# Kernel tuning notes

Measured on AMD Instinct MI355X. Metric: run time of the kernel, lower is better.

## Reference

```python
import math
import jax, jax.numpy as jnp
import numpy as np

BATCH, SEQ, EMBED, HEADS = 2, 2048, 1024, 16
HEAD_DIM = EMBED // HEADS


def setup_inputs() -> dict:
    key = jax.random.key(0)
    k1, k2, k3 = jax.random.split(key, 3)
    scale = 1.0 / math.sqrt(EMBED)  # keep pre-softmax logits in a sane range
    x = jax.random.normal(k1, (BATCH, SEQ, EMBED), dtype=jnp.float32)
    mask = jnp.ones((BATCH, SEQ), dtype=jnp.int32)
    qkv_w = jax.random.normal(k2, (3 * EMBED, EMBED), dtype=jnp.float32) * scale
    out_w = jax.random.normal(k3, (EMBED, EMBED), dtype=jnp.float32) * scale
    out_b = jnp.zeros((EMBED,), dtype=jnp.float32)
    return {"x": x, "mask": mask, "qkv_w": qkv_w, "out_w": out_w, "out_b": out_b}


def reference(x, mask, qkv_w, out_w, out_b):
    b, s, e = x.shape
    # qkv projection (torch Linear: x @ W.T), then split heads
    qkv = (x @ qkv_w.T).reshape(b, s, 3, HEADS, HEAD_DIM)
    q, k, v = qkv[:, :, 0], qkv[:, :, 1], qkv[:, :, 2]  # each [b,s,h,d]
    # full score matrix [b,h,s,s]
    scores = jnp.einsum('bshd,bthd->bhst', q, k) / math.sqrt(HEAD_DIM)
    # mask broadcast over query dim and heads: [b,1,1,s_keys]
    scores = jnp.where(mask[:, None, None, :] == 0, -jnp.inf, scores)
    attn = jax.nn.softmax(scores, axis=-1)
    # dropout is identity in eval mode
    out = jnp.einsum('bhst,bthd->bshd', attn, v).reshape(b, s, e)
    return out @ out_w.T + out_b
```

## Files before the change

### kernel.cpp

```cpp
#include <hip/hip_runtime.h>
#include <hip/hip_bf16.h>

#define BATCH 2
#define SEQ   2048
#define EMBED 1024
#define HEADS 16
#define HDIM  64
#define NBH   (BATCH*HEADS)

typedef __attribute__((ext_vector_type(8))) short short8;
typedef __attribute__((ext_vector_type(4))) float floatx4;
typedef unsigned short u16;
typedef unsigned int   u32;

__device__ __forceinline__ void async_cp16(const void* g, void* l) {
  __builtin_amdgcn_global_load_lds((const __attribute__((address_space(1))) void*)g,
                                   (__attribute__((address_space(3))) void*)l,
                                   16, 0, 0);
}

__device__ __forceinline__ u16 f2b(float f) {
  union { float f; u32 u; } x; x.f = f;
  return (u16)((x.u + 0x7fffu + ((x.u >> 16) & 1u)) >> 16);
}
__device__ __forceinline__ u32 pk2(float a, float b) {
  __hip_bfloat162 t = __float22bfloat162_rn(make_float2(a, b));
  return *reinterpret_cast<u32*>(&t);
}

__global__ __launch_bounds__(256)
void cvt_all(const float* __restrict__ x, const float* __restrict__ wqkv,
             const float* __restrict__ wo,
             u16* __restrict__ xb, u16* __restrict__ wqkvb, u16* __restrict__ wob) {
  const size_t t = (size_t)blockIdx.x * 256 + threadIdx.x;
  const float* src; u16* dst; size_t off;
  if (t < 1048576) { src = x; dst = xb; off = t; }
  else if (t < 1048576 + 786432) { src = wqkv; dst = wqkvb; off = t - 1048576; }
  else { src = wo; dst = wob; off = t - (1048576 + 786432); }
  float4 v = *(const float4*)(src + off * 4);
  ushort4 o;
  o.x = f2b(v.x); o.y = f2b(v.y); o.z = f2b(v.z); o.w = f2b(v.w);
  *(ushort4*)(dst + off * 4) = o;
}

__global__ __launch_bounds__(256, 2)
void qkv_gemm(const u16* __restrict__ X, const u16* __restrict__ W,
              u16* __restrict__ q_ws, u16* __restrict__ k_ws, u16* __restrict__ v_ws) {
  __shared__ u16 As[4][128][8];
  __shared__ u16 Bs[4][128][8];
  const int tid  = threadIdx.x;
  const int lane = tid & 63, wv = tid >> 6;
  const int l15  = lane & 15, quad = lane >> 4;
  const int wm = (wv >> 1) << 6, wn = (wv & 1) << 6;
  const int m0 = blockIdx.y << 7, n0 = blockIdx.x << 7;

  floatx4 acc[4][4];
#pragma unroll
  for (int i = 0; i < 4; ++i)
#pragma unroll
    for (int j = 0; j < 4; ++j) acc[i][j] = {0.f, 0.f, 0.f, 0.f};

  for (int k0 = 0; k0 < EMBED; k0 += 32) {
    __syncthreads();
#pragma unroll
    for (int i = 0; i < 2; ++i) {
      int c = tid + (i << 8);
      int kb = c >> 7, row = c & 127;
      async_cp16(X + (size_t)(m0 + row) * EMBED + k0 + kb * 8, &As[kb][row][0]);
      async_cp16(W + (size_t)(n0 + row) * EMBED + k0 + kb * 8, &Bs[kb][row][0]);
    }
    __syncthreads();

    short8 af[4], bf[4];
#pragma unroll
    for (int t = 0; t < 4; ++t) {
      af[t] = *(const short8*)&As[quad][wm + t * 16 + l15][0];
      bf[t] = *(const short8*)&Bs[quad][wn + t * 16 + l15][0];
    }
#pragma unroll
    for (int i = 0; i < 4; ++i)
#pragma unroll
      for (int j = 0; j < 4; ++j)
        acc[i][j] = __builtin_amdgcn_mfma_f32_16x16x32_bf16(af[i], bf[j], acc[i][j], 0, 0, 0);
  }

#pragma unroll
  for (int i = 0; i < 4; ++i) {
#pragma unroll
    for (int j = 0; j < 4; ++j) {
      int col = n0 + wn + j * 16 + l15;
      int c = col >> 10, hd = col & 1023;
      int h = hd >> 6, d = hd & 63;
      u16* dst = (c == 0) ? q_ws : (c == 1) ? k_ws : v_ws;
#pragma unroll
      for (int r = 0; r < 4; ++r) {
        int m = m0 + wm + i * 16 + quad * 4 + r;
        int b = m >> 11, s = m & 2047;
        dst[(((size_t)(b * HEADS + h)) * SEQ + s) * HDIM + d] = f2b(acc[i][j][r]);
      }
    }
  }
}

__global__ __launch_bounds__(256, 2)
void attn_kernel(const u16* __restrict__ q_ws, const u16* __restrict__ k_ws,
                 const u16* __restrict__ v_ws, const int* __restrict__ mask,
                 u16* __restrict__ ao) {
  __shared__ u16 Ks[8][64][8];
  __shared__ u16 Vt[64][72];
  __shared__ u16 Ps[128][72];
  __shared__ float msk[64];
  __shared__ float abuf[4][32];

  const int tid  = threadIdx.x;
  const int lane = tid & 63, wv = tid >> 6;
  const int l15  = lane & 15, quad = lane >> 4;
  const int bh = blockIdx.y;
  const int b  = bh >> 4, h = bh & 15;
  const int qrw = (blockIdx.x << 7) + (wv << 5);

  const u16* Qb = q_ws + (size_t)bh * SEQ * HDIM;
  const u16* Kb = k_ws + (size_t)bh * SEQ * HDIM;
  const u16* Vb = v_ws + (size_t)bh * SEQ * HDIM;

  short8 qf[2][2];
#pragma unroll
  for (int qh = 0; qh < 2; ++qh)
#pragma unroll
    for (int s = 0; s < 2; ++s) {
      short8 v = *(const short8*)(Qb + (size_t)(qrw + qh * 16 + l15) * HDIM + s * 32 + quad * 8);
#pragma unroll
      for (int e = 0; e < 8; ++e) {
        union { float f; u32 u; } x;
        x.u = ((u32)(u16)v[e]) << 16;
        x.f *= 0.125f;
        v[e] = (short)(x.u >> 16);
      }
      qf[qh][s] = v;
    }

  float m_run[2] = {-1e30f, -1e30f}, l_run[2] = {0.f, 0.f};
  floatx4 O[2][4];
#pragma unroll
  for (int qh = 0; qh < 2; ++qh)
#pragma unroll
    for (int dt = 0; dt < 4; ++dt) O[qh][dt] = {0.f, 0.f, 0.f, 0.f};

  const int p = tid >> 3, d0 = (tid & 7) * 8;
  short8 vr0 = *(const short8*)(Vb + (size_t)(2 * p) * HDIM + d0);
  short8 vr1 = *(const short8*)(Vb + (size_t)(2 * p + 1) * HDIM + d0);

  for (int t0 = 0; t0 < SEQ; t0 += 64) {
    __syncthreads();
#pragma unroll
    for (int i = 0; i < 2; ++i) {
      int c = tid + (i << 8);
      int kb = c >> 6, t = c & 63;
      async_cp16(Kb + (size_t)(t0 + t) * HDIM + kb * 8, &Ks[kb][t][0]);
    }
#pragma unroll
    for (int j = 0; j < 8; ++j) {
      u32 pk = ((u32)(u16)vr0[j]) | (((u32)(u16)vr1[j]) << 16);
      *(u32*)&Vt[d0 + j][2 * p] = pk;
    }
    if (tid < 64) msk[tid] = mask[b * SEQ + t0 + tid] ? 0.f : -1e30f;
    __syncthreads();

    if (t0 + 64 < SEQ) {
      vr0 = *(const short8*)(Vb + (size_t)(t0 + 64 + 2 * p) * HDIM + d0);
      vr1 = *(const short8*)(Vb + (size_t)(t0 + 64 + 2 * p + 1) * HDIM + d0);
    }

    floatx4 sc0[4], sc1[4];
#pragma unroll
    for (int nt = 0; nt < 4; ++nt) {
      sc0[nt] = {0.f, 0.f, 0.f, 0.f};
      sc1[nt] = {0.f, 0.f, 0.f, 0.f};
#pragma unroll
      for (int s = 0; s < 2; ++s) {
        short8 kf = *(const short8*)&Ks[s * 4 + quad][nt * 16 + l15][0];
        sc0[nt] = __builtin_amdgcn_mfma_f32_16x16x32_bf16(kf, qf[0][s], sc0[nt], 0, 0, 0);
        sc1[nt] = __builtin_amdgcn_mfma_f32_16x16x32_bf16(kf, qf[1][s], sc1[nt], 0, 0, 0);
      }
    }

    float mt0 = -1e30f, mt1 = -1e30f;
#pragma unroll
    for (int nt = 0; nt < 4; ++nt) {
      const float4 m4 = *(const float4*)&msk[nt * 16 + quad * 4];
#pragma unroll
      for (int r = 0; r < 4; ++r) {
        float mr = (&m4.x)[r];
        sc0[nt][r] += mr; sc1[nt][r] += mr;
        mt0 = fmaxf(mt0, sc0[nt][r]);
        mt1 = fmaxf(mt1, sc1[nt][r]);
      }
    }
    mt0 = fmaxf(mt0, __shfl_xor(mt0, 16)); mt0 = fmaxf(mt0, __shfl_xor(mt0, 32));
    mt1 = fmaxf(mt1, __shfl_xor(mt1, 16)); mt1 = fmaxf(mt1, __shfl_xor(mt1, 32));

    const float mn0 = fmaxf(m_run[0], mt0), mn1 = fmaxf(m_run[1], mt1);
    const float al0 = __expf(m_run[0] - mn0), al1 = __expf(m_run[1] - mn1);
    m_run[0] = mn0; m_run[1] = mn1;

    float rs0 = 0.f, rs1 = 0.f;
    const int prow0 = (wv << 5) + l15, pcol = quad << 2;
#pragma unroll
    for (int nt = 0; nt < 4; ++nt) {
      float p0[4], p1[4];
#pragma unroll
      for (int r = 0; r < 4; ++r) {
        p0[r] = __expf(sc0[nt][r] - mn0); rs0 += p0[r];
        p1[r] = __expf(sc1[nt][r] - mn1); rs1 += p1[r];
      }
      uint2 w0, w1;
      w0.x = pk2(p0[0], p0[1]); w0.y = pk2(p0[2], p0[3]);
      w1.x = pk2(p1[0], p1[1]); w1.y = pk2(p1[2], p1[3]);
      *(uint2*)&Ps[prow0][nt * 16 + pcol]      = w0;
      *(uint2*)&Ps[prow0 + 16][nt * 16 + pcol] = w1;
    }
    rs0 += __shfl_xor(rs0, 16); rs0 += __shfl_xor(rs0, 32);
    rs1 += __shfl_xor(rs1, 16); rs1 += __shfl_xor(rs1, 32);
    l_run[0] = l_run[0] * al0 + rs0;
    l_run[1] = l_run[1] * al1 + rs1;

    if (quad < 2) abuf[wv][(quad << 4) + l15] = quad ? al1 : al0;
    const float4 a0 = *(const float4*)&abuf[wv][quad << 2];
    const float4 a1 = *(const float4*)&abuf[wv][16 + (quad << 2)];
#pragma unroll
    for (int dt = 0; dt < 4; ++dt)
#pragma unroll
      for (int r = 0; r < 4; ++r) {
        O[0][dt][r] *= (&a0.x)[r];
        O[1][dt][r] *= (&a1.x)[r];
      }

#pragma unroll
    for (int tch = 0; tch < 2; ++tch) {
      short8 pf0 = *(const short8*)&Ps[prow0][tch * 32 + quad * 8];
      short8 pf1 = *(const short8*)&Ps[prow0 + 16][tch * 32 + quad * 8];
#pragma unroll
      for (int dt = 0; dt < 4; ++dt) {
        short8 vf = *(const short8*)&Vt[dt * 16 + l15][tch * 32 + quad * 8];
        O[0][dt] = __builtin_amdgcn_mfma_f32_16x16x32_bf16(pf0, vf, O[0][dt], 0, 0, 0);
        O[1][dt] = __builtin_amdgcn_mfma_f32_16x16x32_bf16(pf1, vf, O[1][dt], 0, 0, 0);
      }
    }
  }

  __syncthreads();
  if (quad < 2) abuf[wv][(quad << 4) + l15] = quad ? l_run[1] : l_run[0];
  const float4 li0 = *(const float4*)&abuf[wv][quad << 2];
  const float4 li1 = *(const float4*)&abuf[wv][16 + (quad << 2)];
#pragma unroll
  for (int qh = 0; qh < 2; ++qh) {
#pragma unroll
    for (int r = 0; r < 4; ++r) {
      float inv = 1.f / (qh ? (&li1.x)[r] : (&li0.x)[r]);
      int srow = qrw + qh * 16 + quad * 4 + r;
#pragma unroll
      for (int dt = 0; dt < 4; ++dt) {
        int d = dt * 16 + l15;
        ao[((size_t)(b * SEQ + srow)) * EMBED + h * 64 + d] = f2b(O[qh][dt][r] * inv);
      }
    }
  }
}

__global__ __launch_bounds__(256, 2)
void proj_gemm(const u16* __restrict__ A, const u16* __restrict__ W,
               const float* __restrict__ bias, float* __restrict__ out) {
  __shared__ u16 As[4][128][8];
  __shared__ u16 Bs[4][64][8];
  const int tid  = threadIdx.x;
  const int lane = tid & 63, wv = tid >> 6;
  const int l15  = lane & 15, quad = lane >> 4;
  const int wm = (wv >> 1) << 6, wn = (wv & 1) << 5;
  const int m0 = blockIdx.y << 7, n0 = blockIdx.x << 6;

  floatx4 acc[4][2];
#pragma unroll
  for (int i = 0; i < 4; ++i)
#pragma unroll
    for (int j = 0; j < 2; ++j) acc[i][j] = {0.f, 0.f, 0.f, 0.f};

  for (int k0 = 0; k0 < EMBED; k0 += 32) {
    __syncthreads();
#pragma unroll
    for (int i = 0; i < 2; ++i) {
      int c = tid + (i << 8);
      int kb = c >> 7, row = c & 127;
      async_cp16(A + (size_t)(m0 + row) * EMBED + k0 + kb * 8, &As[kb][row][0]);
    }
    {
      int kb = tid >> 6, row = tid & 63;
      async_cp16(W + (size_t)(n0 + row) * EMBED + k0 + kb * 8, &Bs[kb][row][0]);
    }
    __syncthreads();

    short8 af[4], bf[2];
#pragma unroll
    for (int t = 0; t < 4; ++t)
      af[t] = *(const short8*)&As[quad][wm + t * 16 + l15][0];
#pragma unroll
    for (int t = 0; t < 2; ++t)
      bf[t] = *(const short8*)&Bs[quad][wn + t * 16 + l15][0];
#pragma unroll
    for (int i = 0; i < 4; ++i)
#pragma unroll
      for (int j = 0; j < 2; ++j)
        acc[i][j] = __builtin_amdgcn_mfma_f32_16x16x32_bf16(af[i], bf[j], acc[i][j], 0, 0, 0);
  }

#pragma unroll
  for (int i = 0; i < 4; ++i) {
#pragma unroll
    for (int j = 0; j < 2; ++j) {
      int col = n0 + wn + j * 16 + l15;
      float bv = bias[col];
#pragma unroll
      for (int r = 0; r < 4; ++r) {
        int m = m0 + wm + i * 16 + quad * 4 + r;
        out[(size_t)m * EMBED + col] = acc[i][j][r] + bv;
      }
    }
  }
}

extern "C" void kernel_launch(void* const* d_in, const int* in_sizes, int n_in,
                              void* d_out, int out_size, void* d_ws, size_t ws_size,
                              hipStream_t stream) {
  const float* x     = (const float*)d_in[0];
  const int*   mask  = (const int*)d_in[1];
  const float* qkv_w = (const float*)d_in[2];
  const float* out_w = (const float*)d_in[3];
  const float* out_b = (const float*)d_in[4];
  float* out = (float*)d_out;

  const size_t per = (size_t)NBH * SEQ * HDIM;
  u16* xb    = (u16*)d_ws;
  u16* wqkvb = xb + 4194304;
  u16* wob   = wqkvb + 3145728;
  u16* q_ws  = wob + 1048576;
  u16* k_ws  = q_ws + per;
  u16* v_ws  = k_ws + per;
  u16* ao    = v_ws + per;

  cvt_all<<<8192, 256, 0, stream>>>(x, qkv_w, out_w, xb, wqkvb, wob);
  qkv_gemm<<<dim3(24, 32), 256, 0, stream>>>(xb, wqkvb, q_ws, k_ws, v_ws);
  attn_kernel<<<dim3(SEQ / 128, NBH), 256, 0, stream>>>(q_ws, k_ws, v_ws, mask, ao);
  proj_gemm<<<dim3(16, 32), 256, 0, stream>>>(ao, wob, out_b, out);
}
```

Before: 254.1 us.

## Shrink attention tile to 16 query rows per wave and transpose PV output

```diff
diff --git a/kernel.cpp b/kernel.cpp
--- a/kernel.cpp
+++ b/kernel.cpp
@@ -102,49 +102,44 @@
   }
 }
 
-__global__ __launch_bounds__(256, 2)
+__global__ __launch_bounds__(256, 4)
 void attn_kernel(const u16* __restrict__ q_ws, const u16* __restrict__ k_ws,
                  const u16* __restrict__ v_ws, const int* __restrict__ mask,
                  u16* __restrict__ ao) {
   __shared__ u16 Ks[8][64][8];
   __shared__ u16 Vt[64][72];
-  __shared__ u16 Ps[128][72];
+  __shared__ u16 Ps[4][16][72];
   __shared__ float msk[64];
-  __shared__ float abuf[4][32];
 
   const int tid  = threadIdx.x;
   const int lane = tid & 63, wv = tid >> 6;
   const int l15  = lane & 15, quad = lane >> 4;
   const int bh = blockIdx.y;
   const int b  = bh >> 4, h = bh & 15;
-  const int qrw = (blockIdx.x << 7) + (wv << 5);
+  const int qrw = (blockIdx.x << 6) + (wv << 4);
 
   const u16* Qb = q_ws + (size_t)bh * SEQ * HDIM;
   const u16* Kb = k_ws + (size_t)bh * SEQ * HDIM;
   const u16* Vb = v_ws + (size_t)bh * SEQ * HDIM;
 
-  short8 qf[2][2];
-#pragma unroll
-  for (int qh = 0; qh < 2; ++qh)
-#pragma unroll
-    for (int s = 0; s < 2; ++s) {
-      short8 v = *(const short8*)(Qb + (size_t)(qrw + qh * 16 + l15) * HDIM + s * 32 + quad * 8);
-#pragma unroll
-      for (int e = 0; e < 8; ++e) {
-        union { float f; u32 u; } x;
-        x.u = ((u32)(u16)v[e]) << 16;
-        x.f *= 0.125f;
-        v[e] = (short)(x.u >> 16);
-      }
-      qf[qh][s] = v;
-    }
-
-  float m_run[2] = {-1e30f, -1e30f}, l_run[2] = {0.f, 0.f};
-  floatx4 O[2][4];
-#pragma unroll
-  for (int qh = 0; qh < 2; ++qh)
-#pragma unroll
-    for (int dt = 0; dt < 4; ++dt) O[qh][dt] = {0.f, 0.f, 0.f, 0.f};
+  short8 qf[2];
+#pragma unroll
+  for (int s = 0; s < 2; ++s) {
+    short8 v = *(const short8*)(Qb + (size_t)(qrw + l15) * HDIM + s * 32 + quad * 8);
+#pragma unroll
+    for (int e = 0; e < 8; ++e) {
+      union { float f; u32 u; } x;
+      x.u = ((u32)(u16)v[e]) << 16;
+      x.f *= 0.125f;
+      v[e] = (short)(x.u >> 16);
+    }
+    qf[s] = v;
+  }
+
+  float m_run = -1e30f, l_run = 0.f;
+  floatx4 O[4];
+#pragma unroll
+  for (int dt = 0; dt < 4; ++dt) O[dt] = {0.f, 0.f, 0.f, 0.f};
 
   const int p = tid >> 3, d0 = (tid & 7) * 8;
   short8 vr0 = *(const short8*)(Vb + (size_t)(2 * p) * HDIM + d0);
@@ -171,99 +166,72 @@
       vr1 = *(const short8*)(Vb + (size_t)(t0 + 64 + 2 * p + 1) * HDIM + d0);
     }
 
-    floatx4 sc0[4], sc1[4];
+    floatx4 sc[4];
 #pragma unroll
     for (int nt = 0; nt < 4; ++nt) {
-      sc0[nt] = {0.f, 0.f, 0.f, 0.f};
-      sc1[nt] = {0.f, 0.f, 0.f, 0.f};
+      sc[nt] = {0.f, 0.f, 0.f, 0.f};
 #pragma unroll
       for (int s = 0; s < 2; ++s) {
         short8 kf = *(const short8*)&Ks[s * 4 + quad][nt * 16 + l15][0];
-        sc0[nt] = __builtin_amdgcn_mfma_f32_16x16x32_bf16(kf, qf[0][s], sc0[nt], 0, 0, 0);
-        sc1[nt] = __builtin_amdgcn_mfma_f32_16x16x32_bf16(kf, qf[1][s], sc1[nt], 0, 0, 0);
-      }
-    }
-
-    float mt0 = -1e30f, mt1 = -1e30f;
+        sc[nt] = __builtin_amdgcn_mfma_f32_16x16x32_bf16(kf, qf[s], sc[nt], 0, 0, 0);
+      }
+    }
+
+    float mt = -1e30f;
 #pragma unroll
     for (int nt = 0; nt < 4; ++nt) {
       const float4 m4 = *(const float4*)&msk[nt * 16 + quad * 4];
 #pragma unroll
       for (int r = 0; r < 4; ++r) {
-        float mr = (&m4.x)[r];
-        sc0[nt][r] += mr; sc1[nt][r] += mr;
-        mt0 = fmaxf(mt0, sc0[nt][r]);
-        mt1 = fmaxf(mt1, sc1[nt][r]);
-      }
-    }
-    mt0 = fmaxf(mt0, __shfl_xor(mt0, 16)); mt0 = fmaxf(mt0, __shfl_xor(mt0, 32));
-    mt1 = fmaxf(mt1, __shfl_xor(mt1, 16)); mt1 = fmaxf(mt1, __shfl_xor(mt1, 32));
-
-    const float mn0 = fmaxf(m_run[0], mt0), mn1 = fmaxf(m_run[1], mt1);
-    const float al0 = __expf(m_run[0] - mn0), al1 = __expf(m_run[1] - mn1);
-    m_run[0] = mn0; m_run[1] = mn1;
-
-    float rs0 = 0.f, rs1 = 0.f;
-    const int prow0 = (wv << 5) + l15, pcol = quad << 2;
+        sc[nt][r] += (&m4.x)[r];
+        mt = fmaxf(mt, sc[nt][r]);
+      }
+    }
+    mt = fmaxf(mt, __shfl_xor(mt, 16));
+    mt = fmaxf(mt, __shfl_xor(mt, 32));
+
+    const float mn = fmaxf(m_run, mt);
+    const float al = __expf(m_run - mn);
+    m_run = mn;
+
+    float rs = 0.f;
 #pragma unroll
     for (int nt = 0; nt < 4; ++nt) {
-      float p0[4], p1[4];
-#pragma unroll
-      for (int r = 0; r < 4; ++r) {
-        p0[r] = __expf(sc0[nt][r] - mn0); rs0 += p0[r];
-        p1[r] = __expf(sc1[nt][r] - mn1); rs1 += p1[r];
-      }
-      uint2 w0, w1;
-      w0.x = pk2(p0[0], p0[1]); w0.y = pk2(p0[2], p0[3]);
-      w1.x = pk2(p1[0], p1[1]); w1.y = pk2(p1[2], p1[3]);
-      *(uint2*)&Ps[prow0][nt * 16 + pcol]      = w0;
-      *(uint2*)&Ps[prow0 + 16][nt * 16 + pcol] = w1;
-    }
-    rs0 += __shfl_xor(rs0, 16); rs0 += __shfl_xor(rs0, 32);
-    rs1 += __shfl_xor(rs1, 16); rs1 += __shfl_xor(rs1, 32);
-    l_run[0] = l_run[0] * al0 + rs0;
-    l_run[1] = l_run[1] * al1 + rs1;
-
-    if (quad < 2) abuf[wv][(quad << 4) + l15] = quad ? al1 : al0;
-    const float4 a0 = *(const float4*)&abuf[wv][quad << 2];
-    const float4 a1 = *(const float4*)&abuf[wv][16 + (quad << 2)];
+      float pv[4];
+#pragma unroll
+      for (int r = 0; r < 4; ++r) { pv[r] = __expf(sc[nt][r] - mn); rs += pv[r]; }
+      uint2 w;
+      w.x = pk2(pv[0], pv[1]); w.y = pk2(pv[2], pv[3]);
+      *(uint2*)&Ps[wv][l15][nt * 16 + (quad << 2)] = w;
+    }
+    rs += __shfl_xor(rs, 16);
+    rs += __shfl_xor(rs, 32);
+    l_run = l_run * al + rs;
+
 #pragma unroll
     for (int dt = 0; dt < 4; ++dt)
 #pragma unroll
-      for (int r = 0; r < 4; ++r) {
-        O[0][dt][r] *= (&a0.x)[r];
-        O[1][dt][r] *= (&a1.x)[r];
-      }
+      for (int r = 0; r < 4; ++r) O[dt][r] *= al;
 
 #pragma unroll
     for (int tch = 0; tch < 2; ++tch) {
-      short8 pf0 = *(const short8*)&Ps[prow0][tch * 32 + quad * 8];
-      short8 pf1 = *(const short8*)&Ps[prow0 + 16][tch * 32 + quad * 8];
+      short8 pf = *(const short8*)&Ps[wv][l15][tch * 32 + quad * 8];
 #pragma unroll
       for (int dt = 0; dt < 4; ++dt) {
         short8 vf = *(const short8*)&Vt[dt * 16 + l15][tch * 32 + quad * 8];
-        O[0][dt] = __builtin_amdgcn_mfma_f32_16x16x32_bf16(pf0, vf, O[0][dt], 0, 0, 0);
-        O[1][dt] = __builtin_amdgcn_mfma_f32_16x16x32_bf16(pf1, vf, O[1][dt], 0, 0, 0);
-      }
-    }
-  }
-
-  __syncthreads();
-  if (quad < 2) abuf[wv][(quad << 4) + l15] = quad ? l_run[1] : l_run[0];
-  const float4 li0 = *(const float4*)&abuf[wv][quad << 2];
-  const float4 li1 = *(const float4*)&abuf[wv][16 + (quad << 2)];
-#pragma unroll
-  for (int qh = 0; qh < 2; ++qh) {
-#pragma unroll
-    for (int r = 0; r < 4; ++r) {
-      float inv = 1.f / (qh ? (&li1.x)[r] : (&li0.x)[r]);
-      int srow = qrw + qh * 16 + quad * 4 + r;
-#pragma unroll
-      for (int dt = 0; dt < 4; ++dt) {
-        int d = dt * 16 + l15;
-        ao[((size_t)(b * SEQ + srow)) * EMBED + h * 64 + d] = f2b(O[qh][dt][r] * inv);
-      }
-    }
+        O[dt] = __builtin_amdgcn_mfma_f32_16x16x32_bf16(vf, pf, O[dt], 0, 0, 0);
+      }
+    }
+  }
+
+  const float inv = 1.f / l_run;
+  const size_t rowbase = ((size_t)(b * SEQ + qrw + l15)) * EMBED + h * 64;
+#pragma unroll
+  for (int dt = 0; dt < 4; ++dt) {
+    uint2 w;
+    w.x = pk2(O[dt][0] * inv, O[dt][1] * inv);
+    w.y = pk2(O[dt][2] * inv, O[dt][3] * inv);
+    *(uint2*)(ao + rowbase + dt * 16 + (quad << 2)) = w;
   }
 }
 
@@ -348,6 +316,6 @@
 
   cvt_all<<<8192, 256, 0, stream>>>(x, qkv_w, out_w, xb, wqkvb, wob);
   qkv_gemm<<<dim3(24, 32), 256, 0, stream>>>(xb, wqkvb, q_ws, k_ws, v_ws);
-  attn_kernel<<<dim3(SEQ / 128, NBH), 256, 0, stream>>>(q_ws, k_ws, v_ws, mask, ao);
+  attn_kernel<<<dim3(SEQ / 64, NBH), 256, 0, stream>>>(q_ws, k_ws, v_ws, mask, ao);
   proj_gemm<<<dim3(16, 32), 256, 0, stream>>>(ao, wob, out_b, out);
 }
```

Measured after the change: 263.0 us. 1.04x slower.
